# Kernel optimization log

Hardware: AMD Instinct MI355X
Metric: run time of the kernel (lower is better)

## Reference

```python
import jax, jax.numpy as jnp
import numpy as np

BETA = 1.0 - 0.01      # 1 - voltage_decay
THRESH = 1.0           # threshold_voltage; theta state is never updated in the
                       # original forward (theta1/theta2 stay at init=0), so the
                       # effective adaptive threshold is THRESH + 0 every step.
ALPHA = 2.0            # snntorch default ATan surrogate alpha

@jax.custom_vjp
def spike_fn(x):
    # Heaviside forward, ATan surrogate backward (snntorch default spike_grad)
    return (x > 0).astype(x.dtype)

def _spike_fwd(x):
    return (x > 0).astype(x.dtype), x

def _spike_bwd(x, g):
    return (g * (ALPHA / 2.0) / (1.0 + (jnp.pi / 2.0 * ALPHA * x) ** 2),)

spike_fn.defvjp(_spike_fwd, _spike_bwd)

def setup_inputs() -> dict:
    key = jax.random.key(0)
    k0, k1, k2 = jax.random.split(key, 3)
    B, T, D, H, A = 128, 32, 6400, 1000, 4
    x = jax.random.normal(k0, (B, T, D), jnp.float32)
    W1 = jax.random.normal(k1, (H, D), jnp.float32) * (1.0 / np.sqrt(D))
    b1 = jnp.zeros((H,), jnp.float32)
    W2 = jax.random.normal(k2, (A, H), jnp.float32) * (1.0 / np.sqrt(H))
    b2 = jnp.zeros((A,), jnp.float32)
    return {"x": x, "W1": W1, "b1": b1, "W2": W2, "b2": b2}

def _lif_step(mem, cur, thr):
    # snntorch Leaky, reset_mechanism='zero':
    #   reset based on PREVIOUS mem crossing threshold (detached),
    #   zeroes the whole new state (leaked mem + input) on reset step.
    reset = jax.lax.stop_gradient((mem > thr).astype(mem.dtype))
    mem_new = (BETA * mem + cur) * (1.0 - reset)
    spk = spike_fn(mem_new - thr)
    return spk, mem_new

def _snn_forward(x, W1, b1, W2, b2):
    B, T, _ = x.shape
    H, A = W1.shape[0], W2.shape[0]

    def step(carry, cur):
        mem1, mem2 = carry
        h1 = cur @ W1.T + b1                 # [B,H]
        spk1, mem1 = _lif_step(mem1, h1, THRESH)
        h2 = spk1 @ W2.T + b2                # [B,A]
        spk2, mem2 = _lif_step(mem2, h2, THRESH)
        return (mem1, mem2), spk2

    init = (jnp.zeros((B, H), x.dtype), jnp.zeros((B, A), x.dtype))
    xt = jnp.swapaxes(x, 0, 1)               # [T,B,D]
    _, spk2_rec = jax.lax.scan(step, init, xt)
    return jnp.swapaxes(spk2_rec, 0, 1)      # [B,T,A]

def reference(x, W1, b1, W2, b2):
    return _snn_forward(x, W1, b1, W2, b2)
```

## Files before the change

### kernel.cpp

```cpp
#include <hip/hip_runtime.h>
#include <hip/hip_bf16.h>

constexpr int Bn = 128;
constexpr int Tn = 32;
constexpr int Dn = 6400;
constexpr int Hn = 1000;
constexpr int An = 4;
constexpr int Mn = Bn * Tn;
constexpr int Npad = 1024;

constexpr int KS = Dn / 32;
constexpr int MC = Mn / 16;
constexpr int NC = Npad / 16;

typedef _Float16 half8 __attribute__((ext_vector_type(8)));
typedef _Float16 half4 __attribute__((ext_vector_type(4)));
typedef float floatx4 __attribute__((ext_vector_type(4)));

constexpr size_t H1_BYTES  = (size_t)Mn * Hn * 4;
constexpr size_t XS_BYTES  = (size_t)Mn * Dn * 2;
constexpr size_t WSp_BYTES = (size_t)Npad * Dn * 2;
constexpr size_t WS_R7     = H1_BYTES + 2 * XS_BYTES + 2 * WSp_BYTES;
constexpr size_t WS_SPLITK = 2 * H1_BYTES + 2 * XS_BYTES + 2 * WSp_BYTES;

__device__ __forceinline__ void async16(const void* g, void* l) {
    __builtin_amdgcn_global_load_lds(
        (const __attribute__((address_space(1))) void*)g,
        (__attribute__((address_space(3))) void*)l, 16, 0, 0);
}

__global__ __launch_bounds__(256)
void cvt2(const float* __restrict__ X, const float* __restrict__ W1,
          _Float16* __restrict__ Xh, _Float16* __restrict__ Xl,
          _Float16* __restrict__ Wh, _Float16* __restrict__ Wl)
{
    constexpr int LD2 = 264;
    __shared__ __align__(16) _Float16 hiS[16][LD2];
    __shared__ __align__(16) _Float16 loS[16][LD2];

    const int tid = threadIdx.x;
    const int lane = tid & 63;
    const int w = tid >> 6;
    const int bx = blockIdx.x;

    const float* src;
    _Float16 *dh, *dl;
    int c4, ks0, crow, nrows;
    if (bx < 256 * 25) {
        c4 = bx & 255; ks0 = (bx >> 8) * 8;
        src = X; dh = Xh; dl = Xl; crow = MC; nrows = 16;
    } else {
        const int b2 = bx - 256 * 25;
        c4 = b2 & 63; ks0 = (b2 >> 6) * 8;
        src = W1; dh = Wh; dl = Wl; crow = NC; nrows = Hn - c4 * 16;
    }

#pragma unroll
    for (int j = 0; j < 4; ++j) {
        const int row = w * 4 + j;
        float4 v = make_float4(0.f, 0.f, 0.f, 0.f);
        if (row < nrows)
            v = *(const float4*)(src + (size_t)(c4 * 16 + row) * Dn + ks0 * 32 + lane * 4);
        half4 hi, lo;
        const float vx = v.x * 16.0f, vy = v.y * 16.0f,
                    vz = v.z * 16.0f, vw = v.w * 16.0f;
        hi[0] = (_Float16)vx; lo[0] = (_Float16)(vx - (float)hi[0]);
        hi[1] = (_Float16)vy; lo[1] = (_Float16)(vy - (float)hi[1]);
        hi[2] = (_Float16)vz; lo[2] = (_Float16)(vz - (float)hi[2]);
        hi[3] = (_Float16)vw; lo[3] = (_Float16)(vw - (float)hi[3]);
        *(half4*)&hiS[row][lane * 4] = hi;
        *(half4*)&loS[row][lane * 4] = lo;
    }
    __syncthreads();

    const int lr = lane & 15, lg = lane >> 4;
#pragma unroll
    for (int q = 0; q < 2; ++q) {
        const int ks = w * 2 + q;
        const size_t cbase = ((size_t)(ks0 + ks) * crow + c4) * 512;
        const half8 h = *(const half8*)&hiS[lr][ks * 32 + lg * 8];
        const half8 l = *(const half8*)&loS[lr][ks * 32 + lg * 8];
        *(half8*)(dh + cbase + lane * 8) = h;
        *(half8*)(dl + cbase + lane * 8) = l;
    }
}

__global__ __launch_bounds__(256, 2)
void gemm_sk2(const _Float16* __restrict__ Xh, const _Float16* __restrict__ Xl,
              const _Float16* __restrict__ Wh, const _Float16* __restrict__ Wl,
              float* __restrict__ H1)
{
    __shared__ __align__(16) _Float16 S[4][16][512];

    const int tid = threadIdx.x;
    const int lane = tid & 63;
    const int w = tid >> 6;
    const int kh = blockIdx.x & 1;
    const int nb = (blockIdx.x >> 1) & 7;
    const int mb = blockIdx.x >> 4;
    const int bm8 = mb * 8;
    const int bn8 = nb * 8;
    const int wm = w & 1;
    const int wn = w >> 1;
    const int ks0 = kh * (KS / 2);
    constexpr int NIT = KS / 2;

    auto issueA = [&](int ks, int buf) {
        _Float16* base = &S[buf][0][0];
#pragma unroll
        for (int r = 0; r < 2; ++r) {
            const int i = w * 2 + r;
            const size_t ga = ((size_t)(ks * MC + bm8 + i)) * 512 + lane * 8;
            async16(Xh + ga, base + (0 + i) * 512);
            async16(Xl + ga, base + (8 + i) * 512);
        }
    };

    const _Float16* bhp = Wh + ((size_t)(ks0 * NC + bn8 + wn * 4)) * 512 + lane * 8;
    const _Float16* blp = Wl + ((size_t)(ks0 * NC + bn8 + wn * 4)) * 512 + lane * 8;
    constexpr size_t BSTEP = (size_t)NC * 512;

    floatx4 acc[4][4] = {};

    half8 bhA[4], blA[4], bhB[4], blB[4];

    issueA(ks0 + 0, 0);
#pragma unroll
    for (int nt = 0; nt < 4; ++nt) {
        bhA[nt] = *(const half8*)(bhp + nt * 512);
        blA[nt] = *(const half8*)(blp + nt * 512);
    }
    issueA(ks0 + 1, 1);

#define SK2_BODY(IT, BUF, BCH, BCL, BNH, BNL)                                   \
    {                                                                           \
        asm volatile("s_waitcnt vmcnt(8)" ::: "memory");                        \
        __builtin_amdgcn_sched_barrier(0);                                      \
        __builtin_amdgcn_s_barrier();                                           \
        __builtin_amdgcn_sched_barrier(0);                                      \
        if ((IT) + 1 < NIT) {                                                   \
            const size_t bo = (size_t)((IT) + 1) * BSTEP;                       \
            _Pragma("unroll")                                                   \
            for (int nt = 0; nt < 4; ++nt) {                                    \
                BNH[nt] = *(const half8*)(bhp + bo + nt * 512);                 \
                BNL[nt] = *(const half8*)(blp + bo + nt * 512);                 \
            }                                                                   \
        }                                                                       \
        __builtin_amdgcn_sched_barrier(0);                                      \
        if ((IT) + 2 < NIT) issueA(ks0 + (IT) + 2, ((IT) + 2) & 3);             \
        __builtin_amdgcn_sched_barrier(0);                                      \
        half8 ah[4], al[4];                                                     \
        _Pragma("unroll")                                                       \
        for (int mt = 0; mt < 4; ++mt) {                                        \
            ah[mt] = *(const half8*)&S[BUF][wm * 4 + mt][lane * 8];             \
            al[mt] = *(const half8*)&S[BUF][8 + wm * 4 + mt][lane * 8];         \
        }                                                                       \
        _Pragma("unroll")                                                       \
        for (int mt = 0; mt < 4; ++mt)                                          \
            _Pragma("unroll")                                                   \
            for (int nt = 0; nt < 4; ++nt)                                      \
                acc[mt][nt] = __builtin_amdgcn_mfma_f32_16x16x32_f16(ah[mt], BCH[nt], acc[mt][nt], 0, 0, 0); \
        _Pragma("unroll")                                                       \
        for (int mt = 0; mt < 4; ++mt)                                          \
            _Pragma("unroll")                                                   \
            for (int nt = 0; nt < 4; ++nt)                                      \
                acc[mt][nt] = __builtin_amdgcn_mfma_f32_16x16x32_f16(ah[mt], BCL[nt], acc[mt][nt], 0, 0, 0); \
        _Pragma("unroll")                                                       \
        for (int mt = 0; mt < 4; ++mt)                                          \
            _Pragma("unroll")                                                   \
            for (int nt = 0; nt < 4; ++nt)                                      \
                acc[mt][nt] = __builtin_amdgcn_mfma_f32_16x16x32_f16(al[mt], BCH[nt], acc[mt][nt], 0, 0, 0); \
    }

    for (int it = 0; it < NIT; it += 4) {
        SK2_BODY(it + 0, 0, bhA, blA, bhB, blB);
        SK2_BODY(it + 1, 1, bhB, blB, bhA, blA);
        SK2_BODY(it + 2, 2, bhA, blA, bhB, blB);
        SK2_BODY(it + 3, 3, bhB, blB, bhA, blA);
    }
#undef SK2_BODY

    float* H1o = H1 + (size_t)kh * ((size_t)Mn * Hn);
    const int fr = lane & 15;
    const int fq = lane >> 4;
#pragma unroll
    for (int nt = 0; nt < 4; ++nt) {
        const int n = nb * 128 + wn * 64 + nt * 16 + fr;
        if (n >= Hn) continue;
#pragma unroll
        for (int mt = 0; mt < 4; ++mt) {
            const int m = mb * 128 + wm * 64 + mt * 16 + fq * 4;
#pragma unroll
            for (int r = 0; r < 4; ++r)
                H1o[(size_t)(m + r) * Hn + n] = acc[mt][nt][r] * (1.0f / 256.0f);
        }
    }
}

constexpr int AH = 0;
constexpr int AL = 8 * 512;
constexpr int BH = 16 * 512;
constexpr int BL = 20 * 512;
constexpr int BUFSZ = 24 * 512;

__global__ __launch_bounds__(256, 2)
void gemm_frag2(const _Float16* __restrict__ Xh, const _Float16* __restrict__ Xl,
                const _Float16* __restrict__ Wh, const _Float16* __restrict__ Wl,
                float* __restrict__ H1)
{
    __shared__ __align__(16) _Float16 S[2 * BUFSZ];

    const int tid = threadIdx.x;
    const int lane = tid & 63;
    const int w = tid >> 6;
    const int nb = blockIdx.x & 15;
    const int mb = blockIdx.x >> 4;
    const int bm4 = mb * 8;
    const int bn4 = nb * 4;
    const int wm = w & 1;
    const int wn = w >> 1;

    auto issue = [&](int ks, int buf) {
        _Float16* base = &S[buf * BUFSZ];
#pragma unroll
        for (int r = 0; r < 2; ++r) {
            const int i = w * 2 + r;
            const size_t ga = ((size_t)(ks * MC + bm4 + i)) * 512 + lane * 8;
            async16(Xh + ga, base + AH + i * 512);
            async16(Xl + ga, base + AL + i * 512);
        }
        const size_t gb = ((size_t)(ks * NC + bn4 + w)) * 512 + lane * 8;
        async16(Wh + gb, base + BH + w * 512);
        async16(Wl + gb, base + BL + w * 512);
    };

    floatx4 acc0[4][2] = {};
    floatx4 acc1[4][2] = {};

    issue(0, 0);
    for (int it = 0; it < KS; ++it) {
        const int buf = it & 1;
        __syncthreads();
        if (it + 1 < KS) issue(it + 1, buf ^ 1);

        const _Float16* base = &S[buf * BUFSZ];
        half8 ah[4], al[4], bh[2], bl[2];
#pragma unroll
        for (int mt = 0; mt < 4; ++mt) {
            ah[mt] = *(const half8*)(base + AH + (wm * 4 + mt) * 512 + lane * 8);
            al[mt] = *(const half8*)(base + AL + (wm * 4 + mt) * 512 + lane * 8);
        }
#pragma unroll
        for (int nt = 0; nt < 2; ++nt) {
            bh[nt] = *(const half8*)(base + BH + (wn * 2 + nt) * 512 + lane * 8);
            bl[nt] = *(const half8*)(base + BL + (wn * 2 + nt) * 512 + lane * 8);
        }
#pragma unroll
        for (int mt = 0; mt < 4; ++mt)
#pragma unroll
            for (int nt = 0; nt < 2; ++nt) {
                acc0[mt][nt] = __builtin_amdgcn_mfma_f32_16x16x32_f16(ah[mt], bh[nt], acc0[mt][nt], 0, 0, 0);
                acc1[mt][nt] = __builtin_amdgcn_mfma_f32_16x16x32_f16(ah[mt], bl[nt], acc1[mt][nt], 0, 0, 0);
                acc1[mt][nt] = __builtin_amdgcn_mfma_f32_16x16x32_f16(al[mt], bh[nt], acc1[mt][nt], 0, 0, 0);
            }
    }

    const int fr = lane & 15;
    const int fq = lane >> 4;
#pragma unroll
    for (int nt = 0; nt < 2; ++nt) {
        const int n = nb * 64 + wn * 32 + nt * 16 + fr;
        if (n >= Hn) continue;
#pragma unroll
        for (int mt = 0; mt < 4; ++mt) {
            const int m = mb * 128 + wm * 64 + mt * 16 + fq * 4;
#pragma unroll
            for (int r = 0; r < 4; ++r)
                H1[(size_t)(m + r) * Hn + n] =
                    (acc0[mt][nt][r] + acc1[mt][nt][r]) * (1.0f / 256.0f);
        }
    }
}

__global__ __launch_bounds__(256, 4)
void gemm_fb(const float* __restrict__ X, const float* __restrict__ W1,
             float* __restrict__ H1)
{
    constexpr int K = Dn;
    constexpr int LD = 72;
    __shared__ __align__(16) _Float16 As[2][64][LD];
    __shared__ __align__(16) _Float16 Bs[2][64][LD];

    const int tid = threadIdx.x;
    const int bm = blockIdx.x * 64;
    const int bn = blockIdx.y * 64;
    const int lane = tid & 63;
    const int wid = tid >> 6;
    const int wm = (wid & 1) * 32;
    const int wn = (wid >> 1) * 32;
    const int fr = lane & 15;
    const int fq = lane >> 4;

    const int row0 = tid >> 3;
    const int row1 = (tid + 256) >> 3;
    const int k8_0 = (tid & 7) * 8;

    float4 rx[2][2], rw[2][2];
    const float zero4[4] = {0.f, 0.f, 0.f, 0.f};

    auto load_tiles = [&](int k0) {
        rx[0][0] = *(const float4*)(X + (size_t)(bm + row0) * K + k0 + k8_0);
        rx[0][1] = *(const float4*)(X + (size_t)(bm + row0) * K + k0 + k8_0 + 4);
        rx[1][0] = *(const float4*)(X + (size_t)(bm + row1) * K + k0 + k8_0);
        rx[1][1] = *(const float4*)(X + (size_t)(bm + row1) * K + k0 + k8_0 + 4);
        const int n0 = bn + row0, n1 = bn + row1;
        if (n0 < Hn) {
            rw[0][0] = *(const float4*)(W1 + (size_t)n0 * K + k0 + k8_0);
            rw[0][1] = *(const float4*)(W1 + (size_t)n0 * K + k0 + k8_0 + 4);
        } else { rw[0][0] = *(const float4*)zero4; rw[0][1] = *(const float4*)zero4; }
        if (n1 < Hn) {
            rw[1][0] = *(const float4*)(W1 + (size_t)n1 * K + k0 + k8_0);
            rw[1][1] = *(const float4*)(W1 + (size_t)n1 * K + k0 + k8_0 + 4);
        } else { rw[1][0] = *(const float4*)zero4; rw[1][1] = *(const float4*)zero4; }
    };

    load_tiles(0);
    floatx4 acc0[2][2] = {};
    floatx4 acc1[2][2] = {};

    for (int k0 = 0; k0 < K; k0 += 64) {
#pragma unroll
        for (int p = 0; p < 2; ++p) {
            const int row = p ? row1 : row0;
            float v[8];
            *(float4*)&v[0] = rx[p][0]; *(float4*)&v[4] = rx[p][1];
            half8 hi, lo;
#pragma unroll
            for (int j = 0; j < 8; ++j) {
                hi[j] = (_Float16)v[j];
                lo[j] = (_Float16)((v[j] - (float)hi[j]) * 4096.0f);
            }
            *(half8*)&As[0][row][k8_0] = hi;
            *(half8*)&As[1][row][k8_0] = lo;

            *(float4*)&v[0] = rw[p][0]; *(float4*)&v[4] = rw[p][1];
#pragma unroll
            for (int j = 0; j < 8; ++j) {
                hi[j] = (_Float16)v[j];
                lo[j] = (_Float16)((v[j] - (float)hi[j]) * 4096.0f);
            }
            *(half8*)&Bs[0][row][k8_0] = hi;
            *(half8*)&Bs[1][row][k8_0] = lo;
        }
        __syncthreads();
        if (k0 + 64 < K) load_tiles(k0 + 64);

#pragma unroll
        for (int c = 0; c < 2; ++c) {
            half8 ahi[2], alo[2], bhi[2], blo[2];
#pragma unroll
            for (int mt = 0; mt < 2; ++mt) {
                ahi[mt] = *(const half8*)&As[0][wm + mt * 16 + fr][c * 32 + fq * 8];
                alo[mt] = *(const half8*)&As[1][wm + mt * 16 + fr][c * 32 + fq * 8];
            }
#pragma unroll
            for (int nt = 0; nt < 2; ++nt) {
                bhi[nt] = *(const half8*)&Bs[0][wn + nt * 16 + fr][c * 32 + fq * 8];
                blo[nt] = *(const half8*)&Bs[1][wn + nt * 16 + fr][c * 32 + fq * 8];
            }
#pragma unroll
            for (int mt = 0; mt < 2; ++mt)
#pragma unroll
                for (int nt = 0; nt < 2; ++nt) {
                    acc0[mt][nt] = __builtin_amdgcn_mfma_f32_16x16x32_f16(ahi[mt], bhi[nt], acc0[mt][nt], 0, 0, 0);
                    acc1[mt][nt] = __builtin_amdgcn_mfma_f32_16x16x32_f16(ahi[mt], blo[nt], acc1[mt][nt], 0, 0, 0);
                    acc1[mt][nt] = __builtin_amdgcn_mfma_f32_16x16x32_f16(alo[mt], bhi[nt], acc1[mt][nt], 0, 0, 0);
                }
        }
        __syncthreads();
    }

#pragma unroll
    for (int nt = 0; nt < 2; ++nt) {
        const int n = bn + wn + nt * 16 + fr;
        if (n >= Hn) continue;
#pragma unroll
        for (int mt = 0; mt < 2; ++mt) {
            const int m = bm + wm + mt * 16 + fq * 4;
#pragma unroll
            for (int r = 0; r < 4; ++r)
                H1[(size_t)(m + r) * Hn + n] =
                    acc0[mt][nt][r] + acc1[mt][nt][r] * (1.0f / 4096.0f);
        }
    }
}

__global__ __launch_bounds__(1024)
void snn_scan(const float* __restrict__ H1, const float* __restrict__ b1,
              const float* __restrict__ W2, const float* __restrict__ b2,
              float* __restrict__ out, int split)
{
    const int b = blockIdx.x;
    const int tid = threadIdx.x;
    const int lane = tid & 63;
    const int wid = tid >> 6;
    const bool act = (tid < Hn);
    constexpr size_t MH = (size_t)Mn * Hn;

    __shared__ float w2s[1024][5];
    __shared__ unsigned smask[1024];
    __shared__ float h2s[Tn][An];

#pragma unroll
    for (int a = 0; a < An; ++a)
        w2s[tid][a] = act ? W2[a * Hn + tid] : 0.f;

    const float b1v = act ? b1[tid] : 0.f;

    float cur[Tn];
#pragma unroll
    for (int t = 0; t < Tn; ++t) {
        const size_t idx = ((size_t)b * Tn + t) * Hn + tid;
        float c = act ? H1[idx] : 0.f;
        if (split && act) c += H1[idx + MH];
        cur[t] = c + b1v;
    }

    unsigned mask = 0;
    float mem1 = 0.f;
#pragma unroll
    for (int t = 0; t < Tn; ++t) {
        const float reset = (mem1 > 1.0f) ? 1.0f : 0.0f;
        mem1 = (0.99f * mem1 + cur[t]) * (1.0f - reset);
        if (mem1 > 1.0f) mask |= (1u << t);
    }
    smask[tid] = act ? mask : 0u;
    __syncthreads();

#pragma unroll
    for (int tt = 0; tt < 2; ++tt) {
        const int t = wid * 2 + tt;
        float p[An] = {0.f, 0.f, 0.f, 0.f};
        for (int h = lane; h < 1024; h += 64) {
            const float g = (smask[h] >> t) & 1u ? 1.0f : 0.0f;
#pragma unroll
            for (int a = 0; a < An; ++a) p[a] += g * w2s[h][a];
        }
#pragma unroll
        for (int off = 32; off > 0; off >>= 1)
#pragma unroll
            for (int a = 0; a < An; ++a) p[a] += __shfl_down(p[a], off, 64);
        if (lane == 0) {
#pragma unroll
            for (int a = 0; a < An; ++a) h2s[t][a] = p[a];
        }
    }
    __syncthreads();

    if (tid < An) {
        const float bias = b2[tid];
        float mem2 = 0.f;
#pragma unroll
        for (int t = 0; t < Tn; ++t) {
            const float h2 = h2s[t][tid] + bias;
            const float reset = (mem2 > 1.0f) ? 1.0f : 0.0f;
            mem2 = (0.99f * mem2 + h2) * (1.0f - reset);
            out[((size_t)b * Tn + t) * An + tid] = (mem2 > 1.0f) ? 1.0f : 0.0f;
        }
    }
}

extern "C" void kernel_launch(void* const* d_in, const int* in_sizes, int n_in,
                              void* d_out, int out_size, void* d_ws, size_t ws_size,
                              hipStream_t stream) {
    const float* x  = (const float*)d_in[0];
    const float* W1 = (const float*)d_in[1];
    const float* b1 = (const float*)d_in[2];
    const float* W2 = (const float*)d_in[3];
    const float* b2 = (const float*)d_in[4];
    float* out = (float*)d_out;

    char* ws = (char*)d_ws;
    float* H1 = (float*)ws;

    if (ws_size >= WS_SPLITK) {
        _Float16* Xh = (_Float16*)(ws + 2 * H1_BYTES);
        _Float16* Xl = (_Float16*)(ws + 2 * H1_BYTES + XS_BYTES);
        _Float16* Wh = (_Float16*)(ws + 2 * H1_BYTES + 2 * XS_BYTES);
        _Float16* Wl = (_Float16*)(ws + 2 * H1_BYTES + 2 * XS_BYTES + WSp_BYTES);

        cvt2<<<256 * 25 + 64 * 25, 256, 0, stream>>>(x, W1, Xh, Xl, Wh, Wl);
        gemm_sk2<<<512, 256, 0, stream>>>(Xh, Xl, Wh, Wl, H1);
        snn_scan<<<Bn, 1024, 0, stream>>>(H1, b1, W2, b2, out, 1);
    } else if (ws_size >= WS_R7) {
        _Float16* Xh = (_Float16*)(ws + H1_BYTES);
        _Float16* Xl = (_Float16*)(ws + H1_BYTES + XS_BYTES);
        _Float16* Wh = (_Float16*)(ws + H1_BYTES + 2 * XS_BYTES);
        _Float16* Wl = (_Float16*)(ws + H1_BYTES + 2 * XS_BYTES + WSp_BYTES);

        cvt2<<<256 * 25 + 64 * 25, 256, 0, stream>>>(x, W1, Xh, Xl, Wh, Wl);
        gemm_frag2<<<512, 256, 0, stream>>>(Xh, Xl, Wh, Wl, H1);
        snn_scan<<<Bn, 1024, 0, stream>>>(H1, b1, W2, b2, out, 0);
    } else {
        dim3 grid(Mn / 64, (Hn + 63) / 64);
        gemm_fb<<<grid, 256, 0, stream>>>(x, W1, H1);
        snn_scan<<<Bn, 1024, 0, stream>>>(H1, b1, W2, b2, out, 0);
    }
}
```

Before: 354.4 us.

## Load A operands directly from global into registers, dropping LDS staging

```diff
diff --git a/kernel.cpp b/kernel.cpp
--- a/kernel.cpp
+++ b/kernel.cpp
@@ -90,8 +90,6 @@
               const _Float16* __restrict__ Wh, const _Float16* __restrict__ Wl,
               float* __restrict__ H1)
 {
-    __shared__ __align__(16) _Float16 S[4][16][512];
-
     const int tid = threadIdx.x;
     const int lane = tid & 63;
     const int w = tid >> 6;
@@ -105,80 +103,60 @@
     const int ks0 = kh * (KS / 2);
     constexpr int NIT = KS / 2;
 
-    auto issueA = [&](int ks, int buf) {
-        _Float16* base = &S[buf][0][0];
-#pragma unroll
-        for (int r = 0; r < 2; ++r) {
-            const int i = w * 2 + r;
-            const size_t ga = ((size_t)(ks * MC + bm8 + i)) * 512 + lane * 8;
-            async16(Xh + ga, base + (0 + i) * 512);
-            async16(Xl + ga, base + (8 + i) * 512);
-        }
-    };
-
+    const _Float16* ahp = Xh + ((size_t)(ks0 * MC + bm8 + wm * 4)) * 512 + lane * 8;
+    const _Float16* alp = Xl + ((size_t)(ks0 * MC + bm8 + wm * 4)) * 512 + lane * 8;
     const _Float16* bhp = Wh + ((size_t)(ks0 * NC + bn8 + wn * 4)) * 512 + lane * 8;
     const _Float16* blp = Wl + ((size_t)(ks0 * NC + bn8 + wn * 4)) * 512 + lane * 8;
+    constexpr size_t ASTEP = (size_t)MC * 512;
     constexpr size_t BSTEP = (size_t)NC * 512;
 
     floatx4 acc[4][4] = {};
 
-    half8 bhA[4], blA[4], bhB[4], blB[4];
-
-    issueA(ks0 + 0, 0);
-#pragma unroll
-    for (int nt = 0; nt < 4; ++nt) {
-        bhA[nt] = *(const half8*)(bhp + nt * 512);
-        blA[nt] = *(const half8*)(blp + nt * 512);
-    }
-    issueA(ks0 + 1, 1);
-
-#define SK2_BODY(IT, BUF, BCH, BCL, BNH, BNL)                                   \
+    half8 ahC[4], alC[4], bhC[4], blC[4];
+    half8 ahN[4], alN[4], bhN[4], blN[4];
+
+#define SK2_LOAD(IT, AH_, AL_, BH_, BL_)                                        \
     {                                                                           \
-        asm volatile("s_waitcnt vmcnt(8)" ::: "memory");                        \
-        __builtin_amdgcn_sched_barrier(0);                                      \
-        __builtin_amdgcn_s_barrier();                                           \
-        __builtin_amdgcn_sched_barrier(0);                                      \
-        if ((IT) + 1 < NIT) {                                                   \
-            const size_t bo = (size_t)((IT) + 1) * BSTEP;                       \
-            _Pragma("unroll")                                                   \
-            for (int nt = 0; nt < 4; ++nt) {                                    \
-                BNH[nt] = *(const half8*)(bhp + bo + nt * 512);                 \
-                BNL[nt] = *(const half8*)(blp + bo + nt * 512);                 \
-            }                                                                   \
+        const size_t ao = (size_t)(IT) * ASTEP;                                 \
+        const size_t bo = (size_t)(IT) * BSTEP;                                 \
+        _Pragma("unroll")                                                       \
+        for (int t = 0; t < 4; ++t) {                                           \
+            AH_[t] = *(const half8*)(ahp + ao + t * 512);                       \
+            AL_[t] = *(const half8*)(alp + ao + t * 512);                       \
+            BH_[t] = *(const half8*)(bhp + bo + t * 512);                       \
+            BL_[t] = *(const half8*)(blp + bo + t * 512);                       \
         }                                                                       \
-        __builtin_amdgcn_sched_barrier(0);                                      \
-        if ((IT) + 2 < NIT) issueA(ks0 + (IT) + 2, ((IT) + 2) & 3);             \
-        __builtin_amdgcn_sched_barrier(0);                                      \
-        half8 ah[4], al[4];                                                     \
-        _Pragma("unroll")                                                       \
-        for (int mt = 0; mt < 4; ++mt) {                                        \
-            ah[mt] = *(const half8*)&S[BUF][wm * 4 + mt][lane * 8];             \
-            al[mt] = *(const half8*)&S[BUF][8 + wm * 4 + mt][lane * 8];         \
-        }                                                                       \
+    }
+
+#define SK2_MFMA(AH_, AL_, BH_, BL_)                                            \
+    {                                                                           \
         _Pragma("unroll")                                                       \
         for (int mt = 0; mt < 4; ++mt)                                          \
             _Pragma("unroll")                                                   \
             for (int nt = 0; nt < 4; ++nt)                                      \
-                acc[mt][nt] = __builtin_amdgcn_mfma_f32_16x16x32_f16(ah[mt], BCH[nt], acc[mt][nt], 0, 0, 0); \
+                acc[mt][nt] = __builtin_amdgcn_mfma_f32_16x16x32_f16(AH_[mt], BH_[nt], acc[mt][nt], 0, 0, 0); \
         _Pragma("unroll")                                                       \
         for (int mt = 0; mt < 4; ++mt)                                          \
             _Pragma("unroll")                                                   \
             for (int nt = 0; nt < 4; ++nt)                                      \
-                acc[mt][nt] = __builtin_amdgcn_mfma_f32_16x16x32_f16(ah[mt], BCL[nt], acc[mt][nt], 0, 0, 0); \
+                acc[mt][nt] = __builtin_amdgcn_mfma_f32_16x16x32_f16(AH_[mt], BL_[nt], acc[mt][nt], 0, 0, 0); \
         _Pragma("unroll")                                                       \
         for (int mt = 0; mt < 4; ++mt)                                          \
             _Pragma("unroll")                                                   \
             for (int nt = 0; nt < 4; ++nt)                                      \
-                acc[mt][nt] = __builtin_amdgcn_mfma_f32_16x16x32_f16(al[mt], BCH[nt], acc[mt][nt], 0, 0, 0); \
-    }
-
-    for (int it = 0; it < NIT; it += 4) {
-        SK2_BODY(it + 0, 0, bhA, blA, bhB, blB);
-        SK2_BODY(it + 1, 1, bhB, blB, bhA, blA);
-        SK2_BODY(it + 2, 2, bhA, blA, bhB, blB);
-        SK2_BODY(it + 3, 3, bhB, blB, bhA, blA);
-    }
-#undef SK2_BODY
+                acc[mt][nt] = __builtin_amdgcn_mfma_f32_16x16x32_f16(AL_[mt], BH_[nt], acc[mt][nt], 0, 0, 0); \
+    }
+
+    SK2_LOAD(0, ahC, alC, bhC, blC);
+
+    for (int it = 0; it < NIT; it += 2) {
+        SK2_LOAD(it + 1, ahN, alN, bhN, blN);
+        SK2_MFMA(ahC, alC, bhC, blC);
+        if (it + 2 < NIT) SK2_LOAD(it + 2, ahC, alC, bhC, blC);
+        SK2_MFMA(ahN, alN, bhN, blN);
+    }
+#undef SK2_LOAD
+#undef SK2_MFMA
 
     float* H1o = H1 + (size_t)kh * ((size_t)Mn * Hn);
     const int fr = lane & 15;
```

New measurement: 368.3 us. 1.04x slower.

## Deepen split-K GEMM pipeline: prefetch A three stages ahead and register double-buffer LDS reads

Applied to the files above, without the earlier changes.

```diff
diff --git a/kernel.cpp b/kernel.cpp
--- a/kernel.cpp
+++ b/kernel.cpp
@@ -122,61 +122,70 @@
 
     floatx4 acc[4][4] = {};
 
-    half8 bhA[4], blA[4], bhB[4], blB[4];
+    half8 ah0[4], al0[4], bh0[4], bl0[4];
+    half8 ah1[4], al1[4], bh1[4], bl1[4];
 
     issueA(ks0 + 0, 0);
+    issueA(ks0 + 1, 1);
 #pragma unroll
     for (int nt = 0; nt < 4; ++nt) {
-        bhA[nt] = *(const half8*)(bhp + nt * 512);
-        blA[nt] = *(const half8*)(blp + nt * 512);
-    }
-    issueA(ks0 + 1, 1);
-
-#define SK2_BODY(IT, BUF, BCH, BCL, BNH, BNL)                                   \
+        bh0[nt] = *(const half8*)(bhp + nt * 512);
+        bl0[nt] = *(const half8*)(blp + nt * 512);
+    }
+    issueA(ks0 + 2, 2);
+    asm volatile("s_waitcnt vmcnt(16)" ::: "memory");
+    __builtin_amdgcn_sched_barrier(0);
+    __builtin_amdgcn_s_barrier();
+    __builtin_amdgcn_sched_barrier(0);
+#pragma unroll
+    for (int mt = 0; mt < 4; ++mt) {
+        ah0[mt] = *(const half8*)&S[0][wm * 4 + mt][lane * 8];
+        al0[mt] = *(const half8*)&S[0][8 + wm * 4 + mt][lane * 8];
+    }
+
+#define SK2_BODY(IT, CAH, CAL, CBH, CBL, NAH, NAL, NBH, NBL)                    \
     {                                                                           \
-        asm volatile("s_waitcnt vmcnt(8)" ::: "memory");                        \
+        asm volatile("s_waitcnt vmcnt(12)" ::: "memory");                       \
         __builtin_amdgcn_sched_barrier(0);                                      \
         __builtin_amdgcn_s_barrier();                                           \
+        __builtin_amdgcn_sched_barrier(0);                                      \
+        _Pragma("unroll")                                                       \
+        for (int mt = 0; mt < 4; ++mt)                                          \
+            _Pragma("unroll")                                                   \
+            for (int nt = 0; nt < 4; ++nt)                                      \
+                acc[mt][nt] = __builtin_amdgcn_mfma_f32_16x16x32_f16(CAH[mt], CBH[nt], acc[mt][nt], 0, 0, 0); \
         __builtin_amdgcn_sched_barrier(0);                                      \
         if ((IT) + 1 < NIT) {                                                   \
             const size_t bo = (size_t)((IT) + 1) * BSTEP;                       \
             _Pragma("unroll")                                                   \
             for (int nt = 0; nt < 4; ++nt) {                                    \
-                BNH[nt] = *(const half8*)(bhp + bo + nt * 512);                 \
-                BNL[nt] = *(const half8*)(blp + bo + nt * 512);                 \
+                NBH[nt] = *(const half8*)(bhp + bo + nt * 512);                 \
+                NBL[nt] = *(const half8*)(blp + bo + nt * 512);                 \
+            }                                                                   \
+            const _Float16* sb = &S[((IT) + 1) & 3][0][0];                      \
+            _Pragma("unroll")                                                   \
+            for (int mt = 0; mt < 4; ++mt) {                                    \
+                NAH[mt] = *(const half8*)(sb + (wm * 4 + mt) * 512 + lane * 8); \
+                NAL[mt] = *(const half8*)(sb + (8 + wm * 4 + mt) * 512 + lane * 8); \
             }                                                                   \
         }                                                                       \
+        if ((IT) + 3 < NIT) issueA(ks0 + (IT) + 3, ((IT) + 3) & 3);             \
         __builtin_amdgcn_sched_barrier(0);                                      \
-        if ((IT) + 2 < NIT) issueA(ks0 + (IT) + 2, ((IT) + 2) & 3);             \
-        __builtin_amdgcn_sched_barrier(0);                                      \
-        half8 ah[4], al[4];                                                     \
-        _Pragma("unroll")                                                       \
-        for (int mt = 0; mt < 4; ++mt) {                                        \
-            ah[mt] = *(const half8*)&S[BUF][wm * 4 + mt][lane * 8];             \
-            al[mt] = *(const half8*)&S[BUF][8 + wm * 4 + mt][lane * 8];         \
-        }                                                                       \
         _Pragma("unroll")                                                       \
         for (int mt = 0; mt < 4; ++mt)                                          \
             _Pragma("unroll")                                                   \
             for (int nt = 0; nt < 4; ++nt)                                      \
-                acc[mt][nt] = __builtin_amdgcn_mfma_f32_16x16x32_f16(ah[mt], BCH[nt], acc[mt][nt], 0, 0, 0); \
+                acc[mt][nt] = __builtin_amdgcn_mfma_f32_16x16x32_f16(CAH[mt], CBL[nt], acc[mt][nt], 0, 0, 0); \
         _Pragma("unroll")                                                       \
         for (int mt = 0; mt < 4; ++mt)                                          \
             _Pragma("unroll")                                                   \
             for (int nt = 0; nt < 4; ++nt)                                      \
-                acc[mt][nt] = __builtin_amdgcn_mfma_f32_16x16x32_f16(ah[mt], BCL[nt], acc[mt][nt], 0, 0, 0); \
-        _Pragma("unroll")                                                       \
-        for (int mt = 0; mt < 4; ++mt)                                          \
-            _Pragma("unroll")                                                   \
-            for (int nt = 0; nt < 4; ++nt)                                      \
-                acc[mt][nt] = __builtin_amdgcn_mfma_f32_16x16x32_f16(al[mt], BCH[nt], acc[mt][nt], 0, 0, 0); \
-    }
-
-    for (int it = 0; it < NIT; it += 4) {
-        SK2_BODY(it + 0, 0, bhA, blA, bhB, blB);
-        SK2_BODY(it + 1, 1, bhB, blB, bhA, blA);
-        SK2_BODY(it + 2, 2, bhA, blA, bhB, blB);
-        SK2_BODY(it + 3, 3, bhB, blB, bhA, blA);
+                acc[mt][nt] = __builtin_amdgcn_mfma_f32_16x16x32_f16(CAL[mt], CBH[nt], acc[mt][nt], 0, 0, 0); \
+    }
+
+    for (int it = 0; it < NIT; it += 2) {
+        SK2_BODY(it + 0, ah0, al0, bh0, bl0, ah1, al1, bh1, bl1);
+        SK2_BODY(it + 1, ah1, al1, bh1, bl1, ah0, al0, bh0, bl0);
     }
 #undef SK2_BODY
 
```

Result: no change. 350.5 us (-1.1%).

## Add three-way split-K GEMM with occupancy 3 and remove B register double-buffering

Applied to the files above, without the earlier changes.

```diff
diff --git a/kernel.cpp b/kernel.cpp
--- a/kernel.cpp
+++ b/kernel.cpp
@@ -22,6 +22,7 @@
 constexpr size_t WSp_BYTES = (size_t)Npad * Dn * 2;
 constexpr size_t WS_R7     = H1_BYTES + 2 * XS_BYTES + 2 * WSp_BYTES;
 constexpr size_t WS_SPLITK = 2 * H1_BYTES + 2 * XS_BYTES + 2 * WSp_BYTES;
+constexpr size_t WS_SK3    = 3 * H1_BYTES + 2 * XS_BYTES + 2 * WSp_BYTES;
 
 __device__ __forceinline__ void async16(const void* g, void* l) {
     __builtin_amdgcn_global_load_lds(
@@ -85,6 +86,119 @@
     }
 }
 
+__global__ __launch_bounds__(256, 3)
+void gemm_sk3(const _Float16* __restrict__ Xh, const _Float16* __restrict__ Xl,
+              const _Float16* __restrict__ Wh, const _Float16* __restrict__ Wl,
+              float* __restrict__ H1)
+{
+    __shared__ __align__(16) _Float16 S[3][16][512];
+
+    const int tid = threadIdx.x;
+    const int lane = tid & 63;
+    const int w = tid >> 6;
+    const int bid = blockIdx.x;
+    const int kh = bid % 3;
+    const int nbmb = bid / 3;
+    const int nb = nbmb & 7;
+    const int mb = nbmb >> 3;
+    const int bm8 = mb * 8;
+    const int bn8 = nb * 8;
+    const int wm = w & 1;
+    const int wn = w >> 1;
+    const int ks0 = kh * 67;
+    const int NIT = (kh == 2) ? 66 : 67;
+
+    auto issueA = [&](int ks, int buf) {
+        _Float16* base = &S[buf][0][0];
+#pragma unroll
+        for (int r = 0; r < 2; ++r) {
+            const int i = w * 2 + r;
+            const size_t ga = ((size_t)(ks * MC + bm8 + i)) * 512 + lane * 8;
+            async16(Xh + ga, base + (0 + i) * 512);
+            async16(Xl + ga, base + (8 + i) * 512);
+        }
+    };
+
+    const _Float16* bhp = Wh + ((size_t)(ks0 * NC + bn8 + wn * 4)) * 512 + lane * 8;
+    const _Float16* blp = Wl + ((size_t)(ks0 * NC + bn8 + wn * 4)) * 512 + lane * 8;
+    constexpr size_t BSTEP = (size_t)NC * 512;
+
+    floatx4 acc[4][4] = {};
+
+    issueA(ks0 + 0, 0);
+    issueA(ks0 + 1, 1);
+
+#define SK3_BODY(IT, BUF, BUFN)                                                 \
+    {                                                                           \
+        asm volatile("s_waitcnt vmcnt(4)" ::: "memory");                        \
+        __builtin_amdgcn_sched_barrier(0);                                      \
+        __builtin_amdgcn_s_barrier();                                           \
+        __builtin_amdgcn_sched_barrier(0);                                      \
+        half8 bh[4], bl[4];                                                     \
+        {                                                                       \
+            const size_t bo = (size_t)(IT) * BSTEP;                             \
+            _Pragma("unroll")                                                   \
+            for (int nt = 0; nt < 4; ++nt) {                                    \
+                bh[nt] = *(const half8*)(bhp + bo + nt * 512);                  \
+                bl[nt] = *(const half8*)(blp + bo + nt * 512);                  \
+            }                                                                   \
+        }                                                                       \
+        __builtin_amdgcn_sched_barrier(0);                                      \
+        if ((IT) + 2 < NIT) issueA(ks0 + (IT) + 2, BUFN);                       \
+        __builtin_amdgcn_sched_barrier(0);                                      \
+        half8 ah[4], al[4];                                                     \
+        _Pragma("unroll")                                                       \
+        for (int mt = 0; mt < 4; ++mt) {                                        \
+            ah[mt] = *(const half8*)&S[BUF][wm * 4 + mt][lane * 8];             \
+            al[mt] = *(const half8*)&S[BUF][8 + wm * 4 + mt][lane * 8];         \
+        }                                                                       \
+        __builtin_amdgcn_s_setprio(1);                                          \
+        _Pragma("unroll")                                                       \
+        for (int mt = 0; mt < 4; ++mt)                                          \
+            _Pragma("unroll")                                                   \
+            for (int nt = 0; nt < 4; ++nt)                                      \
+                acc[mt][nt] = __builtin_amdgcn_mfma_f32_16x16x32_f16(ah[mt], bh[nt], acc[mt][nt], 0, 0, 0); \
+        _Pragma("unroll")                                                       \
+        for (int mt = 0; mt < 4; ++mt)                                          \
+            _Pragma("unroll")                                                   \
+            for (int nt = 0; nt < 4; ++nt)                                      \
+                acc[mt][nt] = __builtin_amdgcn_mfma_f32_16x16x32_f16(ah[mt], bl[nt], acc[mt][nt], 0, 0, 0); \
+        _Pragma("unroll")                                                       \
+        for (int mt = 0; mt < 4; ++mt)                                          \
+            _Pragma("unroll")                                                   \
+            for (int nt = 0; nt < 4; ++nt)                                      \
+                acc[mt][nt] = __builtin_amdgcn_mfma_f32_16x16x32_f16(al[mt], bh[nt], acc[mt][nt], 0, 0, 0); \
+        __builtin_amdgcn_s_setprio(0);                                          \
+    }
+
+    int it = 0;
+    for (; it + 3 <= NIT; it += 3) {
+        SK3_BODY(it + 0, 0, 2);
+        SK3_BODY(it + 1, 1, 0);
+        SK3_BODY(it + 2, 2, 1);
+    }
+    if (it < NIT) {
+        SK3_BODY(it, 0, 2);
+    }
+#undef SK3_BODY
+
+    float* H1o = H1 + (size_t)kh * ((size_t)Mn * Hn);
+    const int fr = lane & 15;
+    const int fq = lane >> 4;
+#pragma unroll
+    for (int nt = 0; nt < 4; ++nt) {
+        const int n = nb * 128 + wn * 64 + nt * 16 + fr;
+        if (n >= Hn) continue;
+#pragma unroll
+        for (int mt = 0; mt < 4; ++mt) {
+            const int m = mb * 128 + wm * 64 + mt * 16 + fq * 4;
+#pragma unroll
+            for (int r = 0; r < 4; ++r)
+                H1o[(size_t)(m + r) * Hn + n] = acc[mt][nt][r] * (1.0f / 256.0f);
+        }
+    }
+}
+
 __global__ __launch_bounds__(256, 2)
 void gemm_sk2(const _Float16* __restrict__ Xh, const _Float16* __restrict__ Xl,
               const _Float16* __restrict__ Wh, const _Float16* __restrict__ Wl,
@@ -122,28 +236,22 @@
 
     floatx4 acc[4][4] = {};
 
-    half8 bhA[4], blA[4], bhB[4], blB[4];
-
     issueA(ks0 + 0, 0);
-#pragma unroll
-    for (int nt = 0; nt < 4; ++nt) {
-        bhA[nt] = *(const half8*)(bhp + nt * 512);
-        blA[nt] = *(const half8*)(blp + nt * 512);
-    }
     issueA(ks0 + 1, 1);
 
-#define SK2_BODY(IT, BUF, BCH, BCL, BNH, BNL)                                   \
+#define SK2_BODY(IT, BUF)                                                       \
     {                                                                           \
-        asm volatile("s_waitcnt vmcnt(8)" ::: "memory");                        \
+        asm volatile("s_waitcnt vmcnt(4)" ::: "memory");                        \
         __builtin_amdgcn_sched_barrier(0);                                      \
         __builtin_amdgcn_s_barrier();                                           \
         __builtin_amdgcn_sched_barrier(0);                                      \
-        if ((IT) + 1 < NIT) {                                                   \
-            const size_t bo = (size_t)((IT) + 1) * BSTEP;                       \
+        half8 bh[4], bl[4];                                                     \
+        {                                                                       \
+            const size_t bo = (size_t)(IT) * BSTEP;                             \
             _Pragma("unroll")                                                   \
             for (int nt = 0; nt < 4; ++nt) {                                    \
-                BNH[nt] = *(const half8*)(bhp + bo + nt * 512);                 \
-                BNL[nt] = *(const half8*)(blp + bo + nt * 512);                 \
+                bh[nt] = *(const half8*)(bhp + bo + nt * 512);                  \
+                bl[nt] = *(const half8*)(blp + bo + nt * 512);                  \
             }                                                                   \
         }                                                                       \
         __builtin_amdgcn_sched_barrier(0);                                      \
@@ -159,24 +267,24 @@
         for (int mt = 0; mt < 4; ++mt)                                          \
             _Pragma("unroll")                                                   \
             for (int nt = 0; nt < 4; ++nt)                                      \
-                acc[mt][nt] = __builtin_amdgcn_mfma_f32_16x16x32_f16(ah[mt], BCH[nt], acc[mt][nt], 0, 0, 0); \
+                acc[mt][nt] = __builtin_amdgcn_mfma_f32_16x16x32_f16(ah[mt], bh[nt], acc[mt][nt], 0, 0, 0); \
         _Pragma("unroll")                                                       \
         for (int mt = 0; mt < 4; ++mt)                                          \
             _Pragma("unroll")                                                   \
             for (int nt = 0; nt < 4; ++nt)                                      \
-                acc[mt][nt] = __builtin_amdgcn_mfma_f32_16x16x32_f16(ah[mt], BCL[nt], acc[mt][nt], 0, 0, 0); \
+                acc[mt][nt] = __builtin_amdgcn_mfma_f32_16x16x32_f16(ah[mt], bl[nt], acc[mt][nt], 0, 0, 0); \
         _Pragma("unroll")                                                       \
         for (int mt = 0; mt < 4; ++mt)                                          \
             _Pragma("unroll")                                                   \
             for (int nt = 0; nt < 4; ++nt)                                      \
-                acc[mt][nt] = __builtin_amdgcn_mfma_f32_16x16x32_f16(al[mt], BCH[nt], acc[mt][nt], 0, 0, 0); \
+                acc[mt][nt] = __builtin_amdgcn_mfma_f32_16x16x32_f16(al[mt], bh[nt], acc[mt][nt], 0, 0, 0); \
     }
 
     for (int it = 0; it < NIT; it += 4) {
-        SK2_BODY(it + 0, 0, bhA, blA, bhB, blB);
-        SK2_BODY(it + 1, 1, bhB, blB, bhA, blA);
-        SK2_BODY(it + 2, 2, bhA, blA, bhB, blB);
-        SK2_BODY(it + 3, 3, bhB, blB, bhA, blA);
+        SK2_BODY(it + 0, 0);
+        SK2_BODY(it + 1, 1);
+        SK2_BODY(it + 2, 2);
+        SK2_BODY(it + 3, 3);
     }
 #undef SK2_BODY
 
@@ -422,7 +530,8 @@
     for (int t = 0; t < Tn; ++t) {
         const size_t idx = ((size_t)b * Tn + t) * Hn + tid;
         float c = act ? H1[idx] : 0.f;
-        if (split && act) c += H1[idx + MH];
+        if (act)
+            for (int s = 1; s <= split; ++s) c += H1[idx + (size_t)s * MH];
         cur[t] = c + b1v;
     }
 
@@ -483,7 +592,16 @@
     char* ws = (char*)d_ws;
     float* H1 = (float*)ws;
 
-    if (ws_size >= WS_SPLITK) {
+    if (ws_size >= WS_SK3) {
+        _Float16* Xh = (_Float16*)(ws + 3 * H1_BYTES);
+        _Float16* Xl = (_Float16*)(ws + 3 * H1_BYTES + XS_BYTES);
+        _Float16* Wh = (_Float16*)(ws + 3 * H1_BYTES + 2 * XS_BYTES);
+        _Float16* Wl = (_Float16*)(ws + 3 * H1_BYTES + 2 * XS_BYTES + WSp_BYTES);
+
+        cvt2<<<256 * 25 + 64 * 25, 256, 0, stream>>>(x, W1, Xh, Xl, Wh, Wl);
+        gemm_sk3<<<768, 256, 0, stream>>>(Xh, Xl, Wh, Wl, H1);
+        snn_scan<<<Bn, 1024, 0, stream>>>(H1, b1, W2, b2, out, 2);
+    } else if (ws_size >= WS_SPLITK) {
         _Float16* Xh = (_Float16*)(ws + 2 * H1_BYTES);
         _Float16* Xl = (_Float16*)(ws + 2 * H1_BYTES + XS_BYTES);
         _Float16* Wh = (_Float16*)(ws + 2 * H1_BYTES + 2 * XS_BYTES);
```

Measured after the change: 378.6 us. 1.07x slower.
